# Optimization experiments

Measured on AMD Instinct MI355X. Metric: run time of the kernel, lower is better.

## Reference

```python
import jax, jax.numpy as jnp
import numpy as np

B, S, HID = 1, 2048, 2048
H = 16
DN, DR, DV = 128, 64, 128          # qk_nope_head_dim, qk_rope_head_dim, v_head_dim
DQ = DN + DR                        # q_head_dim = 192
QLR, KVLR = 1536, 512               # q_lora_rank, kv_lora_rank
MAXP = 32 * 1024
SCALE = DQ ** -0.5
EPS = 1e-6


def rmsnorm(x, w):
    return x * jax.lax.rsqrt(jnp.mean(x * x, axis=-1, keepdims=True) + EPS) * w


def rotate_half(x):
    h = x.shape[-1] // 2
    return jnp.concatenate((-x[..., h:], x[..., :h]), axis=-1)


def interleave_to_half(x):
    # torch: view(b,h,s,d//2,2).transpose(4,3).reshape(b,h,s,d)
    b, h, s, d = x.shape
    return x.reshape(b, h, s, d // 2, 2).transpose(0, 1, 2, 4, 3).reshape(b, h, s, d)


def setup_inputs() -> dict:
    key = jax.random.key(0)
    ks = jax.random.split(key, 8)
    def w(k, shape):
        fan_in = shape[-1]
        return jax.random.normal(k, shape, jnp.float32) * (fan_in ** -0.5)
    inp = {
        "hidden_states": jax.random.normal(ks[0], (B, S, HID), jnp.float32),
        "q_a_w": w(ks[1], (QLR, HID)),
        "q_a_ln": jnp.ones((QLR,), jnp.float32),
        "q_b_w": w(ks[2], (H * DQ, QLR)),
        "kv_a_w": w(ks[3], (KVLR + DR, HID)),
        "kv_a_ln": jnp.ones((KVLR,), jnp.float32),
        "kv_b_w": w(ks[4], (H * (DN + DV), KVLR)),
        "o_w": w(ks[5], (HID, H * DV)),
    }
    # rotary tables, seq_len = 32k
    inv_freq = 1.0 / (10000.0 ** (np.arange(0, DR, 2, dtype=np.float32) / DR))
    t = np.arange(MAXP, dtype=np.float32)
    freqs = np.outer(t, inv_freq)
    emb = np.concatenate((freqs, freqs), axis=-1)
    inp["cos"] = jnp.asarray(np.cos(emb), jnp.float32)
    inp["sin"] = jnp.asarray(np.sin(emb), jnp.float32)
    # bool mask, True = masked (causal)
    inp["attention_mask"] = jnp.triu(jnp.ones((S, S), bool), 1)[None, None]
    inp["position_ids"] = jnp.arange(S, dtype=jnp.int64 if jax.config.jax_enable_x64 else jnp.int32)[None].repeat(B, 0)
    return inp


def reference(hidden_states, q_a_w, q_a_ln, q_b_w, kv_a_w, kv_a_ln, kv_b_w, o_w,
              cos, sin, attention_mask, position_ids):
    b, s, _ = hidden_states.shape
    # low-rank Q: q_b(LN(q_a(x)))
    q = rmsnorm(hidden_states @ q_a_w.T, q_a_ln) @ q_b_w.T         # [b,s,H*DQ]
    q = q.reshape(b, s, H, DQ).transpose(0, 2, 1, 3)               # [b,H,s,DQ]
    q_nope, q_pe = q[..., :DN], q[..., DN:]
    # compressed KV + decoupled rope key
    ckv = hidden_states @ kv_a_w.T                                  # [b,s,KVLR+DR]
    compressed_kv, k_pe = ckv[..., :KVLR], ckv[..., KVLR:]
    k_pe = k_pe.reshape(b, s, 1, DR).transpose(0, 2, 1, 3)          # [b,1,s,DR]
    kv = rmsnorm(compressed_kv, kv_a_ln) @ kv_b_w.T                 # [b,s,H*(DN+DV)]
    kv = kv.reshape(b, s, H, DN + DV).transpose(0, 2, 1, 3)         # [b,H,s,DN+DV]
    k_nope, value_states = kv[..., :DN], kv[..., DN:]
    # rotary with interleaved->half reorder on the rope slice only
    cos_p = cos[position_ids][:, None]                              # [b,1,s,DR]
    sin_p = sin[position_ids][:, None]
    q_pe = interleave_to_half(q_pe)
    k_pe = interleave_to_half(k_pe)
    q_pe = q_pe * cos_p + rotate_half(q_pe) * sin_p
    k_pe = k_pe * cos_p + rotate_half(k_pe) * sin_p
    query_states = jnp.concatenate((q_nope, q_pe), axis=-1)         # [b,H,s,DQ]
    key_states = jnp.concatenate(
        (k_nope, jnp.broadcast_to(k_pe, (b, H, s, DR))), axis=-1)   # [b,H,s,DQ]
    # manual attention
    scores = jnp.einsum("bhqd,bhkd->bhqk", query_states, key_states) * SCALE
    scores = jnp.where(attention_mask, jnp.float32(-10000.0), scores)
    attn = jax.nn.softmax(scores.astype(jnp.float32), axis=-1).astype(query_states.dtype)
    attn_out = jnp.einsum("bhqk,bhkd->bhqd", attn, value_states)    # [b,H,s,DV]
    attn_out = attn_out.transpose(0, 2, 1, 3).reshape(b, s, H * DV)
    return attn_out @ o_w.T                                         # [b,s,HID]
```

## Files before the change

### kernel.cpp

```cpp
#include <hip/hip_runtime.h>
#include <stdint.h>

typedef unsigned short u16;
typedef __attribute__((ext_vector_type(8))) short short8;
typedef __attribute__((ext_vector_type(4))) float f32x4;
typedef __attribute__((ext_vector_type(4))) unsigned short ushort4_t;
typedef __attribute__((ext_vector_type(4))) float float4_t;

#define DEV_INLINE __device__ __forceinline__

DEV_INLINE u16 f2bf(float f) {
    union { float f; unsigned u; } x; x.f = f;
    unsigned u = x.u;
    unsigned r = (u + 0x7FFFu + ((u >> 16) & 1u)) >> 16;
    return (u16)r;
}

DEV_INLINE float fexp2(float x) {
    float r;
    asm("v_exp_f32 %0, %1" : "=v"(r) : "v"(x));
    return r;
}

DEV_INLINE unsigned cvtpk_bf16(float lo, float hi) {
    unsigned r;
    asm("v_cvt_pk_bf16_f32 %0, %1, %2" : "=v"(r) : "v"(lo), "v"(hi));
    return r;
}

template <int CTRL>
DEV_INLINE float dppmaxf(float x) {
    union { float f; int i; } u; u.f = x;
    int y = __builtin_amdgcn_update_dpp(u.i, u.i, CTRL, 0xf, 0xf, true);
    union { int i; float f; } v; v.i = y;
    return fmaxf(x, v.f);
}

DEV_INLINE float dpp_xor1(float x) {
    union { float f; int i; } u; u.f = x;
    int y = __builtin_amdgcn_update_dpp(u.i, u.i, 0xB1, 0xf, 0xf, true);
    union { int i; float f; } v; v.i = y;
    return v.f;
}

DEV_INLINE float rmax16(float x) {
    x = dppmaxf<0xB1>(x);
    x = dppmaxf<0x4E>(x);
    x = dppmaxf<0x141>(x);
    x = dppmaxf<0x140>(x);
    return x;
}

__global__ void conv_all(const float* __restrict__ s0, u16* __restrict__ d0, long e0,
                         const float* __restrict__ s1, u16* __restrict__ d1, long e1,
                         const float* __restrict__ s2, u16* __restrict__ d2, long e2,
                         const float* __restrict__ s3, u16* __restrict__ d3, long e3,
                         const float* __restrict__ s4, u16* __restrict__ d4, long e4,
                         const float* __restrict__ s5, u16* __restrict__ d5, long e5,
                         int rows_valid, int cols4) {
    long i = (long)blockIdx.x * 256 + threadIdx.x;
    if (i >= e5) return;
    if (i >= e4) {
        long j = i - e4;
        long row = j / cols4;
        ushort4_t o; o.x = 0; o.y = 0; o.z = 0; o.w = 0;
        if (row < rows_valid) {
            float4_t v = ((const float4_t*)s5)[j];
            o.x = f2bf(v.x); o.y = f2bf(v.y); o.z = f2bf(v.z); o.w = f2bf(v.w);
        }
        ((ushort4_t*)d5)[j] = o;
        return;
    }
    const float* s; u16* d; long base;
    if      (i < e0) { s = s0; d = d0; base = 0; }
    else if (i < e1) { s = s1; d = d1; base = e0; }
    else if (i < e2) { s = s2; d = d2; base = e1; }
    else if (i < e3) { s = s3; d = d3; base = e2; }
    else             { s = s4; d = d4; base = e3; }
    long j = i - base;
    float4_t v = ((const float4_t*)s)[j];
    ushort4_t o;
    o.x = f2bf(v.x); o.y = f2bf(v.y); o.z = f2bf(v.z); o.w = f2bf(v.w);
    ((ushort4_t*)d)[j] = o;
}

#define BK 32

DEV_INLINE void gload16(const u16* g, u16* l) {
    __builtin_amdgcn_global_load_lds((const __attribute__((address_space(1))) unsigned int*)g,
                                     (__attribute__((address_space(3))) unsigned int*)l,
                                     16, 0, 0);
}

template <typename OT>
__global__ __launch_bounds__(256) void gemm64_db(const u16* __restrict__ A, const u16* __restrict__ B,
                                                 OT* __restrict__ C, int M, int N, int K) {
    __shared__ u16 As[2][64 * BK];
    __shared__ u16 Bs[2][128 * BK];
    const int tid = threadIdx.x;
    const int wid = tid >> 6, lane = tid & 63;
    const int lm = lane & 15, lk = lane >> 4;
    const long bm = (long)blockIdx.y * 64, bn = (long)blockIdx.x * 128;

    f32x4 acc[4][2] = {};

    const int rowS = lane >> 2;
    const int colS = ((lane & 3) ^ ((lane >> 3) & 3)) * 8;
    const int cs = (lm >> 1) & 3;
    const u16* Ag = A + (bm + wid * 16 + rowS) * (long)K + colS;
    const u16* Bg = B + (bn + wid * 32 + rowS) * (long)K + colS;
    const int aoff = wid * 16 * BK;
    const int boff = wid * 32 * BK;

    gload16(Ag, &As[0][aoff]);
    gload16(Bg, &Bs[0][boff]);
    gload16(Bg + 16 * (long)K, &Bs[0][boff + 16 * BK]);
    __syncthreads();

    int cur = 0;
    for (int k0 = 0; k0 < K; k0 += BK) {
        if (k0 + BK < K) {
            gload16(Ag + k0 + BK, &As[cur ^ 1][aoff]);
            gload16(Bg + k0 + BK, &Bs[cur ^ 1][boff]);
            gload16(Bg + 16 * (long)K + k0 + BK, &Bs[cur ^ 1][boff + 16 * BK]);
        }
        short8 af[4], bfr[2];
#pragma unroll
        for (int m = 0; m < 4; ++m)
            af[m] = *(const short8*)&As[cur][(m * 16 + lm) * BK + (lk ^ cs) * 8];
#pragma unroll
        for (int n = 0; n < 2; ++n)
            bfr[n] = *(const short8*)&Bs[cur][(wid * 32 + n * 16 + lm) * BK + (lk ^ cs) * 8];
#pragma unroll
        for (int m = 0; m < 4; ++m)
#pragma unroll
            for (int n = 0; n < 2; ++n)
                acc[m][n] = __builtin_amdgcn_mfma_f32_16x16x32_bf16(af[m], bfr[n], acc[m][n], 0, 0, 0);
        __syncthreads();
        cur ^= 1;
    }

#pragma unroll
    for (int m = 0; m < 4; ++m)
#pragma unroll
        for (int n = 0; n < 2; ++n)
#pragma unroll
            for (int r = 0; r < 4; ++r) {
                long idx = (bm + m * 16 + lk * 4 + r) * (long)N + bn + wid * 32 + n * 16 + lm;
                if constexpr (sizeof(OT) == 4) C[idx] = acc[m][n][r];
                else                           C[idx] = f2bf(acc[m][n][r]);
            }
}

__global__ __launch_bounds__(256) void gemm_qkv(const u16* __restrict__ qnA, const u16* __restrict__ qbB,
                                                const u16* __restrict__ kvnA, const u16* __restrict__ kvbB,
                                                u16* __restrict__ Qb, u16* __restrict__ Kb, u16* __restrict__ Vt,
                                                const int* __restrict__ pos,
                                                const float* __restrict__ cosT, const float* __restrict__ sinT) {
    __shared__ u16 SMEM[12288];
    u16* As = SMEM;
    u16* Bs = SMEM + 4096;
    const int tid = threadIdx.x;
    const int wid = tid >> 6, lane = tid & 63;
    const int lm = lane & 15, lk = lane >> 4;

    const bool isq = blockIdx.x < 768;
    const int gx = isq ? blockIdx.x : blockIdx.x - 768;
    const int nb = isq ? 24 : 32;
    const int K  = isq ? 1536 : 512;
    const u16* A = isq ? qnA : kvnA;
    const u16* B = isq ? qbB : kvbB;
    const long bn = (long)(gx % nb) * 128;
    const long bm = (long)(gx / nb) * 64;

    f32x4 acc[4][2] = {};

    const int rowS = lane >> 2;
    const int colS = ((lane & 3) ^ ((lane >> 3) & 3)) * 8;
    const int cs = (lm >> 1) & 3;
    const u16* Ag = A + (bm + wid * 16 + rowS) * (long)K + colS;
    const u16* Bg = B + (bn + wid * 32 + rowS) * (long)K + colS;
    const int aoff = wid * 16 * BK;
    const int boff = wid * 32 * BK;

    gload16(Ag, &As[aoff]);
    gload16(Bg, &Bs[boff]);
    gload16(Bg + 16 * (long)K, &Bs[boff + 16 * BK]);
    __syncthreads();

    int cur = 0;
    for (int k0 = 0; k0 < K; k0 += BK) {
        if (k0 + BK < K) {
            gload16(Ag + k0 + BK, &As[(cur ^ 1) * 2048 + aoff]);
            gload16(Bg + k0 + BK, &Bs[(cur ^ 1) * 4096 + boff]);
            gload16(Bg + 16 * (long)K + k0 + BK, &Bs[(cur ^ 1) * 4096 + boff + 16 * BK]);
        }
        short8 af[4], bfr[2];
#pragma unroll
        for (int m = 0; m < 4; ++m)
            af[m] = *(const short8*)&As[cur * 2048 + (m * 16 + lm) * BK + (lk ^ cs) * 8];
#pragma unroll
        for (int n = 0; n < 2; ++n)
            bfr[n] = *(const short8*)&Bs[cur * 4096 + (wid * 32 + n * 16 + lm) * BK + (lk ^ cs) * 8];
#pragma unroll
        for (int m = 0; m < 4; ++m)
#pragma unroll
            for (int n = 0; n < 2; ++n)
                acc[m][n] = __builtin_amdgcn_mfma_f32_16x16x32_bf16(af[m], bfr[n], acc[m][n], 0, 0, 0);
        __syncthreads();
        cur ^= 1;
    }

    if (isq) {
#pragma unroll
        for (int n = 0; n < 2; ++n) {
            const int c = (int)bn + wid * 32 + n * 16 + lm;
            const int h = c / 192;
            const int d = c - h * 192;
            const bool pe = (d >= 128);
            const int t = (d - 128) >> 1;
#pragma unroll
            for (int m = 0; m < 4; ++m)
#pragma unroll
                for (int r = 0; r < 4; ++r) {
                    const long row = bm + m * 16 + lk * 4 + r;
                    float own = acc[m][n][r];
                    float par = dpp_xor1(own);
                    float val = own;
                    if (pe) {
                        long p = pos[row];
                        float cc = cosT[p * 64 + t];
                        float ss = sinT[p * 64 + t];
                        val = (d & 1) ? own * cc + par * ss : own * cc - par * ss;
                    }
                    Qb[((long)h * 2048 + row) * 192 + d] = f2bf(val);
                }
        }
    } else {
        const int hh = (gx & 31) >> 1;
        const bool isV = (gx & 1) != 0;
        if (!isV) {
#pragma unroll
            for (int m = 0; m < 4; ++m)
#pragma unroll
                for (int n = 0; n < 2; ++n)
#pragma unroll
                    for (int r = 0; r < 4; ++r)
                        Kb[((long)hh * 2048 + bm + m * 16 + lk * 4 + r) * 192 + wid * 32 + n * 16 + lm]
                            = f2bf(acc[m][n][r]);
        } else {
            __syncthreads();
            u16* Ls = SMEM;
#pragma unroll
            for (int n = 0; n < 2; ++n) {
                int d = wid * 32 + n * 16 + lm;
                int swz = ((d >> 3) & 7) << 3;
#pragma unroll
                for (int m = 0; m < 4; ++m)
#pragma unroll
                    for (int r = 0; r < 4; ++r) {
                        int row = m * 16 + lk * 4 + r;
                        Ls[d * 72 + (row ^ swz)] = f2bf(acc[m][n][r]);
                    }
            }
            __syncthreads();
#pragma unroll
            for (int i = 0; i < 8; ++i) {
                int u = i * 256 + tid;
                int d = u >> 4, s4 = (u & 15) * 4;
                int swz = ((d >> 3) & 7) << 3;
                ushort4_t v;
                v.x = Ls[d * 72 + ((s4 + 0) ^ swz)]; v.y = Ls[d * 72 + ((s4 + 1) ^ swz)];
                v.z = Ls[d * 72 + ((s4 + 2) ^ swz)]; v.w = Ls[d * 72 + ((s4 + 3) ^ swz)];
                *(ushort4_t*)(Vt + ((long)hh * 128 + d) * 2048 + bm + s4) = v;
            }
        }
    }
}

__global__ __launch_bounds__(256) void norm_rope(const float* __restrict__ qkva,
                                                 const float* __restrict__ q_ln,
                                                 const float* __restrict__ kv_ln,
                                                 u16* __restrict__ qn, u16* __restrict__ kvn,
                                                 const int* __restrict__ pos,
                                                 const float* __restrict__ cosT,
                                                 const float* __restrict__ sinT,
                                                 u16* __restrict__ Kb) {
    const int b = blockIdx.x, tid = threadIdx.x;
    if (b < 4096) {
        const bool isq = b < 2048;
        const int row = isq ? b : b - 2048;
        const int ncols = isq ? 1536 : 512;
        const float* x = qkva + (long)row * 2176 + (isq ? 0 : 1536);
        const float* w = isq ? q_ln : kv_ln;
        u16* out = isq ? (qn + (long)row * 1536) : (kvn + (long)row * 512);
        float ss = 0.f;
        for (int c = tid; c < ncols; c += 256) { float v = x[c]; ss = fmaf(v, v, ss); }
#pragma unroll
        for (int off = 32; off > 0; off >>= 1) ss += __shfl_down(ss, off);
        __shared__ float part[4];
        if ((tid & 63) == 0) part[tid >> 6] = ss;
        __syncthreads();
        float tot = part[0] + part[1] + part[2] + part[3];
        float rs = rsqrtf(tot / (float)ncols + 1e-6f);
        for (int c = tid; c < ncols; c += 256) out[c] = f2bf(x[c] * rs * w[c]);
    } else {
        int idx = (b - 4096) * 256 + tid;
        int s = idx >> 5, j = idx & 31;
        long p = pos[s];
        const float* row = qkva + (long)s * 2176 + 2048;
        float x0 = row[2 * j], x1 = row[2 * j + 1];
        float c0 = cosT[p * 64 + j], s0 = sinT[p * 64 + j];
        u16 o0 = f2bf(x0 * c0 - x1 * s0);
        u16 o1 = f2bf(x1 * c0 + x0 * s0);
#pragma unroll
        for (int h = 0; h < 16; ++h) {
            u16* kr = Kb + ((long)h * 2048 + s) * 192 + 128;
            kr[2 * j] = o0; kr[2 * j + 1] = o1;
        }
    }
}

__global__ __launch_bounds__(512) void attn_fwd(const u16* __restrict__ Qb, const u16* __restrict__ Kb,
                                                const u16* __restrict__ Vt, u16* __restrict__ Ao) {
    __shared__ __align__(16) char smem[51712];

    const int b = blockIdx.x;
    const int u = b & 255;
    const int h = (u & 7) * 2 + ((u >> 3) & 1);
    const int bq = u >> 4;
    const int qi = (b < 256) ? bq : 31 - bq;
    const int tid = threadIdx.x;
    const int wid = tid >> 6, lane = tid & 63;
    const int lm = lane & 15, lk = lane >> 4;
    const int s = wid >> 2, wp = wid & 3;
    const int t256 = tid & 255;

    u16* KsS = (u16*)smem + s * 6144;
    u16* VsS = (u16*)(smem + 24576) + s * 4096;
    u16* PsW = (u16*)(smem + 40960) + wid * 640;
    float* ML = (float*)(smem + 51200);
    float* Ob = (float*)smem;

    const u16* Kh = Kb + (long)h * 2048 * 192;
    const u16* Vh = Vt + (long)h * 128 * 2048;

    short8 bones = {};
    if (lm == 0) {
#pragma unroll
        for (int j = 0; j < 8; ++j) bones[j] = (short)0x3F80;
    }
    const float C2 = 0.104117548f;

    const int q0 = qi * 64;
    const int nt = 2 * qi + 2;
    const int niter = qi + 1;

    short8 qf[6];
    const u16* qbase = Qb + ((long)h * 2048 + q0 + wp * 16 + lm) * 192;
#pragma unroll
    for (int kf = 0; kf < 6; ++kf) qf[kf] = *(const short8*)(qbase + kf * 32 + lk * 8);

    f32x4 o[8] = {};
    f32x4 o9 = {};
    float mrow[4] = {-1e30f, -1e30f, -1e30f, -1e30f};

    short8 kreg[3], vreg[2];
    {
        const long k0 = s * 32;
#pragma unroll
        for (int i = 0; i < 3; ++i) {
            int idx = i * 256 + t256; int r = idx / 24, c = (idx % 24) * 8;
            kreg[i] = *(const short8*)(Kh + (k0 + r) * 192 + c);
        }
#pragma unroll
        for (int i = 0; i < 2; ++i) {
            int idx = i * 256 + t256; int dv = idx >> 2, kvb = idx & 3;
            vreg[i] = *(const short8*)(Vh + (long)dv * 2048 + k0 + kvb * 8);
        }
#pragma unroll
        for (int i = 0; i < 3; ++i) {
            int idx = i * 256 + t256; int r = idx / 24, c8 = idx % 24;
            *(short8*)&KsS[r * 192 + ((c8 ^ (r & 7)) << 3)] = kreg[i];
        }
#pragma unroll
        for (int i = 0; i < 2; ++i) {
            int idx = i * 256 + t256; int dv = idx >> 2, kvb = idx & 3;
            *(short8*)&VsS[kvb * 1024 + ((dv * 8) ^ (kvb * 16))] = vreg[i];
        }
    }
    __syncthreads();

    for (int it = 0; it < niter; ++it) {
        const int ts = 2 * it + s;
        const int k0 = ts * 32;
        const bool more = (it + 1 < niter);

        if (more) {
            const long k0n = (long)(ts + 2) * 32;
#pragma unroll
            for (int i = 0; i < 3; ++i) {
                int idx = i * 256 + t256; int r = idx / 24, c = (idx % 24) * 8;
                kreg[i] = *(const short8*)(Kh + (k0n + r) * 192 + c);
            }
#pragma unroll
            for (int i = 0; i < 2; ++i) {
                int idx = i * 256 + t256; int dv = idx >> 2, kvb = idx & 3;
                vreg[i] = *(const short8*)(Vh + (long)dv * 2048 + k0n + kvb * 8);
            }
        }

        f32x4 sfr[2] = {};
#pragma unroll
        for (int n = 0; n < 2; ++n)
#pragma unroll
            for (int kf = 0; kf < 6; ++kf) {
                short8 kb = *(const short8*)&KsS[(n * 16 + lm) * 192 + (((kf * 4 + lk) ^ (lm & 7)) << 3)];
                sfr[n] = __builtin_amdgcn_mfma_f32_16x16x32_bf16(qf[kf], kb, sfr[n], 0, 0, 0);
            }

        float sv[2][4];
        const bool bt = (ts >= nt - 2);
#pragma unroll
        for (int n = 0; n < 2; ++n)
#pragma unroll
            for (int r = 0; r < 4; ++r) {
                float val = sfr[n][r] * C2;
                if (bt && (k0 + n * 16 + lm > q0 + wp * 16 + lk * 4 + r)) val = -1e30f;
                sv[n][r] = val;
            }

        float pmax[4];
#pragma unroll
        for (int r = 0; r < 4; ++r)
            pmax[r] = rmax16(fmaxf(sv[0][r], sv[1][r]));
        bool need = (pmax[0] > mrow[0] + 8.f) || (pmax[1] > mrow[1] + 8.f) ||
                    (pmax[2] > mrow[2] + 8.f) || (pmax[3] > mrow[3] + 8.f);
        if (__any(need)) {
#pragma unroll
            for (int r = 0; r < 4; ++r) {
                float mnew = fmaxf(mrow[r], pmax[r]);
                float alpha = fexp2(mrow[r] - mnew);
                mrow[r] = mnew;
#pragma unroll
                for (int d = 0; d < 8; ++d) o[d][r] *= alpha;
                o9[r] *= alpha;
            }
        }
#pragma unroll
        for (int n = 0; n < 2; ++n) {
            float p0 = fexp2(sv[n][0] - mrow[0]);
            float p1 = fexp2(sv[n][1] - mrow[1]);
            float p2 = fexp2(sv[n][2] - mrow[2]);
            float p3 = fexp2(sv[n][3] - mrow[3]);
            unsigned pk01 = cvtpk_bf16(p0, p1);
            unsigned pk23 = cvtpk_bf16(p2, p3);
            int rb = (lk * 4) * 40 + n * 16 + lm;
            PsW[rb]       = (u16)pk01;
            PsW[rb + 40]  = (u16)(pk01 >> 16);
            PsW[rb + 80]  = (u16)pk23;
            PsW[rb + 120] = (u16)(pk23 >> 16);
        }

        short8 pf = *(const short8*)&PsW[lm * 40 + lk * 8];
#pragma unroll
        for (int d = 0; d < 8; ++d) {
            short8 vf = *(const short8*)&VsS[lk * 1024 + (((d * 16 + lm) * 8) ^ (lk * 16))];
            o[d] = __builtin_amdgcn_mfma_f32_16x16x32_bf16(pf, vf, o[d], 0, 0, 0);
        }
        o9 = __builtin_amdgcn_mfma_f32_16x16x32_bf16(pf, bones, o9, 0, 0, 0);

        __syncthreads();
        if (more) {
#pragma unroll
            for (int i = 0; i < 3; ++i) {
                int idx = i * 256 + t256; int r = idx / 24, c8 = idx % 24;
                *(short8*)&KsS[r * 192 + ((c8 ^ (r & 7)) << 3)] = kreg[i];
            }
#pragma unroll
            for (int i = 0; i < 2; ++i) {
                int idx = i * 256 + t256; int dv = idx >> 2, kvb = idx & 3;
                *(short8*)&VsS[kvb * 1024 + ((dv * 8) ^ (kvb * 16))] = vreg[i];
            }
        }
        __syncthreads();
    }

    if (s == 1) {
#pragma unroll
        for (int d = 0; d < 8; ++d)
#pragma unroll
            for (int r = 0; r < 4; ++r)
                Ob[(wp * 16 + lk * 4 + r) * 128 + d * 16 + lm] = o[d][r];
        if (lm == 0) {
#pragma unroll
            for (int r = 0; r < 4; ++r) {
                int row = wp * 16 + lk * 4 + r;
                ML[row * 2 + 0] = mrow[r];
                ML[row * 2 + 1] = o9[r];
            }
        }
    }
    __syncthreads();
    if (s == 0) {
        float e0[4], e1[4], invl[4];
#pragma unroll
        for (int r = 0; r < 4; ++r) {
            int row = wp * 16 + lk * 4 + r;
            float m1 = ML[row * 2 + 0];
            float l1 = ML[row * 2 + 1];
            float l0 = __shfl(o9[r], lane & 48);
            float M = fmaxf(mrow[r], m1);
            e0[r] = fexp2(mrow[r] - M);
            e1[r] = fexp2(m1 - M);
            invl[r] = 1.f / (l0 * e0[r] + l1 * e1[r]);
        }
#pragma unroll
        for (int d = 0; d < 8; ++d)
#pragma unroll
            for (int r = 0; r < 4; ++r) {
                int row = wp * 16 + lk * 4 + r;
                float val = (o[d][r] * e0[r] +
                             Ob[row * 128 + d * 16 + lm] * e1[r]) * invl[r];
                Ao[((long)q0 + row) * 2048 + h * 128 + d * 16 + lm] = f2bf(val);
            }
    }
}

extern "C" void kernel_launch(void* const* d_in, const int* in_sizes, int n_in,
                              void* d_out, int out_size, void* d_ws, size_t ws_size,
                              hipStream_t stream) {
    (void)in_sizes; (void)n_in; (void)out_size; (void)ws_size;
    const float* hidden  = (const float*)d_in[0];
    const float* q_a_w   = (const float*)d_in[1];
    const float* q_a_ln  = (const float*)d_in[2];
    const float* q_b_w   = (const float*)d_in[3];
    const float* kv_a_w  = (const float*)d_in[4];
    const float* kv_a_ln = (const float*)d_in[5];
    const float* kv_b_w  = (const float*)d_in[6];
    const float* o_w     = (const float*)d_in[7];
    const float* cosT    = (const float*)d_in[8];
    const float* sinT    = (const float*)d_in[9];
    const int*   pos     = (const int*)d_in[11];

    char* ws = (char*)d_ws;
    u16* o_w_bf   = (u16*)(ws + 0);
    u16* qb_w_bf  = (u16*)(ws + 8388608);
    u16* kvb_w_bf = (u16*)(ws + 17825792);
    u16* qn_bf    = (u16*)(ws + 22020096);
    u16* kvn_bf   = (u16*)(ws + 28311552);
    u16* Qb       = (u16*)(ws + 30408704);
    u16* Kb       = (u16*)(ws + 42991616);
    u16* Vt       = (u16*)(ws + 55574528);
    u16* aout_bf  = (u16*)(ws + 63963136);
    u16*   hid_bf    = (u16*)(ws + 72351744);
    u16*   qkva_w_bf = (u16*)(ws + 80740352);
    float* qkva_f    = (float*)(ws + 89653248);

    conv_all<<<19200, 256, 0, stream>>>(
        hidden, hid_bf,                 1048576L,
        q_a_w,  qkva_w_bf,              1835008L,
        q_b_w,  qb_w_bf,                3014656L,
        kv_b_w, kvb_w_bf,               3538944L,
        o_w,    o_w_bf,                 4587520L,
        kv_a_w, qkva_w_bf + 1536L*2048, 4915200L,
        576, 512);

    gemm64_db<float><<<dim3(17, 32), 256, 0, stream>>>(hid_bf, qkva_w_bf, qkva_f, 2048, 2176, 2048);

    norm_rope<<<4352, 256, 0, stream>>>(qkva_f, q_a_ln, kv_a_ln, qn_bf, kvn_bf, pos, cosT, sinT, Kb);

    gemm_qkv<<<1792, 256, 0, stream>>>(qn_bf, qb_w_bf, kvn_bf, kvb_w_bf, Qb, Kb, Vt, pos, cosT, sinT);

    attn_fwd<<<512, 512, 0, stream>>>(Qb, Kb, Vt, aout_bf);

    gemm64_db<float><<<dim3(16, 32), 256, 0, stream>>>(aout_bf, o_w_bf, (float*)d_out, 2048, 2048, 2048);
}
```

Measured before the change: 224.2 us.

## Restructure attention into 4-way KV split with paired causal q-tiles per block

The attention kernel now launches 256 blocks, and each block handles two q-tiles (qi and 31-qi) one after the other to balance causal work. Each block splits the KV range four ways, and each wave computes 32 query rows so every loaded K/V fragment feeds two MFMAs. The four partial softmax states are combined through a two-level tree in shared memory. This raises LDS use to about 101 KB per block, which likely limits a CU to one resident block and adds extra reduction syncs.

New measurement: 310.4 us, median of 2. 38.5% more time.

```diff
diff --git a/kernel.cpp b/kernel.cpp
--- a/kernel.cpp
+++ b/kernel.cpp
@@ -323,24 +323,24 @@
 
 __global__ __launch_bounds__(512) void attn_fwd(const u16* __restrict__ Qb, const u16* __restrict__ Kb,
                                                 const u16* __restrict__ Vt, u16* __restrict__ Ao) {
-    __shared__ __align__(16) char smem[51712];
+    __shared__ __align__(16) char smem[103424];
 
     const int b = blockIdx.x;
-    const int u = b & 255;
-    const int h = (u & 7) * 2 + ((u >> 3) & 1);
-    const int bq = u >> 4;
-    const int qi = (b < 256) ? bq : 31 - bq;
+    const int h = (b & 7) * 2 + ((b >> 3) & 1);
+    const int pi = b >> 4;
     const int tid = threadIdx.x;
     const int wid = tid >> 6, lane = tid & 63;
     const int lm = lane & 15, lk = lane >> 4;
-    const int s = wid >> 2, wp = wid & 3;
-    const int t256 = tid & 255;
-
-    u16* KsS = (u16*)smem + s * 6144;
-    u16* VsS = (u16*)(smem + 24576) + s * 4096;
-    u16* PsW = (u16*)(smem + 40960) + wid * 640;
-    float* ML = (float*)(smem + 51200);
-    float* Ob = (float*)smem;
+    const int s = wid >> 1, wq = wid & 1;
+    const int t128 = tid & 127;
+
+    u16* KsS = (u16*)(smem + s * 20480);
+    u16* VsS = (u16*)(smem + s * 20480 + 12288);
+    u16* PsW = (u16*)(smem + 81920) + wid * 1280;
+    float* MLa = (float*)(smem + 102400);
+    float* MLb = (float*)(smem + 102912);
+    float* BUF0 = (float*)smem;
+    float* BUF1 = (float*)(smem + 32768);
 
     const u16* Kh = Kb + (long)h * 2048 * 192;
     const u16* Vh = Vt + (long)h * 128 * 2048;
@@ -352,178 +352,266 @@
     }
     const float C2 = 0.104117548f;
 
-    const int q0 = qi * 64;
-    const int nt = 2 * qi + 2;
-    const int niter = qi + 1;
-
-    short8 qf[6];
-    const u16* qbase = Qb + ((long)h * 2048 + q0 + wp * 16 + lm) * 192;
-#pragma unroll
-    for (int kf = 0; kf < 6; ++kf) qf[kf] = *(const short8*)(qbase + kf * 32 + lk * 8);
-
-    f32x4 o[8] = {};
-    f32x4 o9 = {};
-    float mrow[4] = {-1e30f, -1e30f, -1e30f, -1e30f};
-
-    short8 kreg[3], vreg[2];
-    {
-        const long k0 = s * 32;
-#pragma unroll
-        for (int i = 0; i < 3; ++i) {
-            int idx = i * 256 + t256; int r = idx / 24, c = (idx % 24) * 8;
-            kreg[i] = *(const short8*)(Kh + (k0 + r) * 192 + c);
-        }
-#pragma unroll
-        for (int i = 0; i < 2; ++i) {
-            int idx = i * 256 + t256; int dv = idx >> 2, kvb = idx & 3;
-            vreg[i] = *(const short8*)(Vh + (long)dv * 2048 + k0 + kvb * 8);
-        }
-#pragma unroll
-        for (int i = 0; i < 3; ++i) {
-            int idx = i * 256 + t256; int r = idx / 24, c8 = idx % 24;
-            *(short8*)&KsS[r * 192 + ((c8 ^ (r & 7)) << 3)] = kreg[i];
-        }
-#pragma unroll
-        for (int i = 0; i < 2; ++i) {
-            int idx = i * 256 + t256; int dv = idx >> 2, kvb = idx & 3;
-            *(short8*)&VsS[kvb * 1024 + ((dv * 8) ^ (kvb * 16))] = vreg[i];
-        }
-    }
-    __syncthreads();
-
-    for (int it = 0; it < niter; ++it) {
-        const int ts = 2 * it + s;
-        const int k0 = ts * 32;
-        const bool more = (it + 1 < niter);
-
-        if (more) {
-            const long k0n = (long)(ts + 2) * 32;
-#pragma unroll
-            for (int i = 0; i < 3; ++i) {
-                int idx = i * 256 + t256; int r = idx / 24, c = (idx % 24) * 8;
-                kreg[i] = *(const short8*)(Kh + (k0n + r) * 192 + c);
-            }
-#pragma unroll
-            for (int i = 0; i < 2; ++i) {
-                int idx = i * 256 + t256; int dv = idx >> 2, kvb = idx & 3;
-                vreg[i] = *(const short8*)(Vh + (long)dv * 2048 + k0n + kvb * 8);
-            }
-        }
-
-        f32x4 sfr[2] = {};
-#pragma unroll
-        for (int n = 0; n < 2; ++n)
-#pragma unroll
-            for (int kf = 0; kf < 6; ++kf) {
-                short8 kb = *(const short8*)&KsS[(n * 16 + lm) * 192 + (((kf * 4 + lk) ^ (lm & 7)) << 3)];
-                sfr[n] = __builtin_amdgcn_mfma_f32_16x16x32_bf16(qf[kf], kb, sfr[n], 0, 0, 0);
-            }
-
-        float sv[2][4];
-        const bool bt = (ts >= nt - 2);
-#pragma unroll
-        for (int n = 0; n < 2; ++n)
-#pragma unroll
-            for (int r = 0; r < 4; ++r) {
-                float val = sfr[n][r] * C2;
-                if (bt && (k0 + n * 16 + lm > q0 + wp * 16 + lk * 4 + r)) val = -1e30f;
-                sv[n][r] = val;
-            }
-
-        float pmax[4];
-#pragma unroll
-        for (int r = 0; r < 4; ++r)
-            pmax[r] = rmax16(fmaxf(sv[0][r], sv[1][r]));
-        bool need = (pmax[0] > mrow[0] + 8.f) || (pmax[1] > mrow[1] + 8.f) ||
-                    (pmax[2] > mrow[2] + 8.f) || (pmax[3] > mrow[3] + 8.f);
-        if (__any(need)) {
-#pragma unroll
-            for (int r = 0; r < 4; ++r) {
-                float mnew = fmaxf(mrow[r], pmax[r]);
-                float alpha = fexp2(mrow[r] - mnew);
-                mrow[r] = mnew;
-#pragma unroll
-                for (int d = 0; d < 8; ++d) o[d][r] *= alpha;
-                o9[r] *= alpha;
-            }
-        }
-#pragma unroll
-        for (int n = 0; n < 2; ++n) {
-            float p0 = fexp2(sv[n][0] - mrow[0]);
-            float p1 = fexp2(sv[n][1] - mrow[1]);
-            float p2 = fexp2(sv[n][2] - mrow[2]);
-            float p3 = fexp2(sv[n][3] - mrow[3]);
-            unsigned pk01 = cvtpk_bf16(p0, p1);
-            unsigned pk23 = cvtpk_bf16(p2, p3);
-            int rb = (lk * 4) * 40 + n * 16 + lm;
-            PsW[rb]       = (u16)pk01;
-            PsW[rb + 40]  = (u16)(pk01 >> 16);
-            PsW[rb + 80]  = (u16)pk23;
-            PsW[rb + 120] = (u16)(pk23 >> 16);
-        }
-
-        short8 pf = *(const short8*)&PsW[lm * 40 + lk * 8];
-#pragma unroll
-        for (int d = 0; d < 8; ++d) {
-            short8 vf = *(const short8*)&VsS[lk * 1024 + (((d * 16 + lm) * 8) ^ (lk * 16))];
-            o[d] = __builtin_amdgcn_mfma_f32_16x16x32_bf16(pf, vf, o[d], 0, 0, 0);
-        }
-        o9 = __builtin_amdgcn_mfma_f32_16x16x32_bf16(pf, bones, o9, 0, 0, 0);
-
-        __syncthreads();
-        if (more) {
-#pragma unroll
-            for (int i = 0; i < 3; ++i) {
-                int idx = i * 256 + t256; int r = idx / 24, c8 = idx % 24;
-                *(short8*)&KsS[r * 192 + ((c8 ^ (r & 7)) << 3)] = kreg[i];
-            }
-#pragma unroll
-            for (int i = 0; i < 2; ++i) {
-                int idx = i * 256 + t256; int dv = idx >> 2, kvb = idx & 3;
-                *(short8*)&VsS[kvb * 1024 + ((dv * 8) ^ (kvb * 16))] = vreg[i];
-            }
-        }
-        __syncthreads();
-    }
-
-    if (s == 1) {
-#pragma unroll
-        for (int d = 0; d < 8; ++d)
-#pragma unroll
-            for (int r = 0; r < 4; ++r)
-                Ob[(wp * 16 + lk * 4 + r) * 128 + d * 16 + lm] = o[d][r];
-        if (lm == 0) {
-#pragma unroll
-            for (int r = 0; r < 4; ++r) {
-                int row = wp * 16 + lk * 4 + r;
-                ML[row * 2 + 0] = mrow[r];
-                ML[row * 2 + 1] = o9[r];
-            }
-        }
-    }
-    __syncthreads();
-    if (s == 0) {
-        float e0[4], e1[4], invl[4];
-#pragma unroll
-        for (int r = 0; r < 4; ++r) {
-            int row = wp * 16 + lk * 4 + r;
-            float m1 = ML[row * 2 + 0];
-            float l1 = ML[row * 2 + 1];
-            float l0 = __shfl(o9[r], lane & 48);
-            float M = fmaxf(mrow[r], m1);
-            e0[r] = fexp2(mrow[r] - M);
-            e1[r] = fexp2(m1 - M);
-            invl[r] = 1.f / (l0 * e0[r] + l1 * e1[r]);
-        }
-#pragma unroll
-        for (int d = 0; d < 8; ++d)
-#pragma unroll
-            for (int r = 0; r < 4; ++r) {
-                int row = wp * 16 + lk * 4 + r;
-                float val = (o[d][r] * e0[r] +
-                             Ob[row * 128 + d * 16 + lm] * e1[r]) * invl[r];
-                Ao[((long)q0 + row) * 2048 + h * 128 + d * 16 + lm] = f2bf(val);
-            }
+    for (int half = 0; half < 2; ++half) {
+        const int qi = half ? (31 - pi) : pi;
+        const int q0 = qi * 64;
+        const int nt = 2 * (qi + 1);
+        const int L = (nt + 3) >> 2;
+
+        short8 qf[2][6];
+#pragma unroll
+        for (int mg = 0; mg < 2; ++mg) {
+            const u16* qbase = Qb + ((long)h * 2048 + q0 + wq * 32 + mg * 16 + lm) * 192;
+#pragma unroll
+            for (int kf = 0; kf < 6; ++kf) qf[mg][kf] = *(const short8*)(qbase + kf * 32 + lk * 8);
+        }
+
+        f32x4 o[2][8] = {};
+        f32x4 o9[2] = {};
+        float mrow[2][4] = {{-1e30f, -1e30f, -1e30f, -1e30f}, {-1e30f, -1e30f, -1e30f, -1e30f}};
+
+        short8 kreg[6], vreg[4];
+        {
+            const bool act0 = (s < nt);
+            const long k0 = (long)s * 32;
+            if (act0) {
+#pragma unroll
+                for (int i = 0; i < 6; ++i) {
+                    int idx = i * 128 + t128; int r = idx / 24, c = (idx % 24) * 8;
+                    kreg[i] = *(const short8*)(Kh + (k0 + r) * 192 + c);
+                }
+#pragma unroll
+                for (int i = 0; i < 4; ++i) {
+                    int idx = i * 128 + t128; int dv = idx >> 2, kvb = idx & 3;
+                    vreg[i] = *(const short8*)(Vh + (long)dv * 2048 + k0 + kvb * 8);
+                }
+#pragma unroll
+                for (int i = 0; i < 6; ++i) {
+                    int idx = i * 128 + t128; int r = idx / 24, c8 = idx % 24;
+                    *(short8*)&KsS[r * 192 + ((c8 ^ (r & 7)) << 3)] = kreg[i];
+                }
+#pragma unroll
+                for (int i = 0; i < 4; ++i) {
+                    int idx = i * 128 + t128; int dv = idx >> 2, kvb = idx & 3;
+                    *(short8*)&VsS[kvb * 1024 + ((dv * 8) ^ (kvb * 16))] = vreg[i];
+                }
+            }
+        }
+        __syncthreads();
+
+        for (int it = 0; it < L; ++it) {
+            const int ts = 4 * it + s;
+            const int k0 = ts * 32;
+            const bool active = (ts < nt);
+            const int ts_n = ts + 4;
+            const bool next_act = (ts_n < nt);
+
+            if (next_act) {
+                const long k0n = (long)ts_n * 32;
+#pragma unroll
+                for (int i = 0; i < 6; ++i) {
+                    int idx = i * 128 + t128; int r = idx / 24, c = (idx % 24) * 8;
+                    kreg[i] = *(const short8*)(Kh + (k0n + r) * 192 + c);
+                }
+#pragma unroll
+                for (int i = 0; i < 4; ++i) {
+                    int idx = i * 128 + t128; int dv = idx >> 2, kvb = idx & 3;
+                    vreg[i] = *(const short8*)(Vh + (long)dv * 2048 + k0n + kvb * 8);
+                }
+            }
+
+            if (active) {
+                f32x4 sfr[2][2] = {};
+#pragma unroll
+                for (int kf = 0; kf < 6; ++kf)
+#pragma unroll
+                    for (int n = 0; n < 2; ++n) {
+                        short8 kb = *(const short8*)&KsS[(n * 16 + lm) * 192 + (((kf * 4 + lk) ^ (lm & 7)) << 3)];
+#pragma unroll
+                        for (int mg = 0; mg < 2; ++mg)
+                            sfr[mg][n] = __builtin_amdgcn_mfma_f32_16x16x32_bf16(qf[mg][kf], kb, sfr[mg][n], 0, 0, 0);
+                    }
+
+                float sv[2][2][4];
+                const bool bt = (ts >= nt - 2);
+#pragma unroll
+                for (int mg = 0; mg < 2; ++mg)
+#pragma unroll
+                    for (int n = 0; n < 2; ++n)
+#pragma unroll
+                        for (int r = 0; r < 4; ++r) {
+                            float val = sfr[mg][n][r] * C2;
+                            if (bt && (k0 + n * 16 + lm > q0 + wq * 32 + mg * 16 + lk * 4 + r)) val = -1e30f;
+                            sv[mg][n][r] = val;
+                        }
+
+                float pmax[2][4];
+#pragma unroll
+                for (int mg = 0; mg < 2; ++mg)
+#pragma unroll
+                    for (int r = 0; r < 4; ++r)
+                        pmax[mg][r] = rmax16(fmaxf(sv[mg][0][r], sv[mg][1][r]));
+                bool need = false;
+#pragma unroll
+                for (int mg = 0; mg < 2; ++mg)
+#pragma unroll
+                    for (int r = 0; r < 4; ++r) need = need || (pmax[mg][r] > mrow[mg][r] + 8.f);
+                if (__any(need)) {
+#pragma unroll
+                    for (int mg = 0; mg < 2; ++mg)
+#pragma unroll
+                        for (int r = 0; r < 4; ++r) {
+                            float mnew = fmaxf(mrow[mg][r], pmax[mg][r]);
+                            float alpha = fexp2(mrow[mg][r] - mnew);
+                            mrow[mg][r] = mnew;
+#pragma unroll
+                            for (int d = 0; d < 8; ++d) o[mg][d][r] *= alpha;
+                            o9[mg][r] *= alpha;
+                        }
+                }
+#pragma unroll
+                for (int mg = 0; mg < 2; ++mg)
+#pragma unroll
+                    for (int n = 0; n < 2; ++n) {
+                        float p0 = fexp2(sv[mg][n][0] - mrow[mg][0]);
+                        float p1 = fexp2(sv[mg][n][1] - mrow[mg][1]);
+                        float p2 = fexp2(sv[mg][n][2] - mrow[mg][2]);
+                        float p3 = fexp2(sv[mg][n][3] - mrow[mg][3]);
+                        unsigned pk01 = cvtpk_bf16(p0, p1);
+                        unsigned pk23 = cvtpk_bf16(p2, p3);
+                        int rb = (mg * 16 + lk * 4) * 40 + n * 16 + lm;
+                        PsW[rb]       = (u16)pk01;
+                        PsW[rb + 40]  = (u16)(pk01 >> 16);
+                        PsW[rb + 80]  = (u16)pk23;
+                        PsW[rb + 120] = (u16)(pk23 >> 16);
+                    }
+
+                short8 pf0 = *(const short8*)&PsW[lm * 40 + lk * 8];
+                short8 pf1 = *(const short8*)&PsW[(16 + lm) * 40 + lk * 8];
+#pragma unroll
+                for (int d = 0; d < 8; ++d) {
+                    short8 vf = *(const short8*)&VsS[lk * 1024 + (((d * 16 + lm) * 8) ^ (lk * 16))];
+                    o[0][d] = __builtin_amdgcn_mfma_f32_16x16x32_bf16(pf0, vf, o[0][d], 0, 0, 0);
+                    o[1][d] = __builtin_amdgcn_mfma_f32_16x16x32_bf16(pf1, vf, o[1][d], 0, 0, 0);
+                }
+                o9[0] = __builtin_amdgcn_mfma_f32_16x16x32_bf16(pf0, bones, o9[0], 0, 0, 0);
+                o9[1] = __builtin_amdgcn_mfma_f32_16x16x32_bf16(pf1, bones, o9[1], 0, 0, 0);
+            }
+
+            __syncthreads();
+            if (next_act) {
+#pragma unroll
+                for (int i = 0; i < 6; ++i) {
+                    int idx = i * 128 + t128; int r = idx / 24, c8 = idx % 24;
+                    *(short8*)&KsS[r * 192 + ((c8 ^ (r & 7)) << 3)] = kreg[i];
+                }
+#pragma unroll
+                for (int i = 0; i < 4; ++i) {
+                    int idx = i * 128 + t128; int dv = idx >> 2, kvb = idx & 3;
+                    *(short8*)&VsS[kvb * 1024 + ((dv * 8) ^ (kvb * 16))] = vreg[i];
+                }
+            }
+            __syncthreads();
+        }
+
+        if (s >= 2) {
+            float* B = (s == 2) ? BUF0 : BUF1;
+            float* ML = (s == 2) ? MLa : MLb;
+#pragma unroll
+            for (int mg = 0; mg < 2; ++mg)
+#pragma unroll
+                for (int d = 0; d < 8; ++d)
+#pragma unroll
+                    for (int r = 0; r < 4; ++r)
+                        B[(wq * 32 + mg * 16 + lk * 4 + r) * 128 + d * 16 + lm] = o[mg][d][r];
+            if (lm == 0) {
+#pragma unroll
+                for (int mg = 0; mg < 2; ++mg)
+#pragma unroll
+                    for (int r = 0; r < 4; ++r) {
+                        int row = wq * 32 + mg * 16 + lk * 4 + r;
+                        ML[row * 2 + 0] = mrow[mg][r];
+                        ML[row * 2 + 1] = o9[mg][r];
+                    }
+            }
+        }
+        __syncthreads();
+        if (s <= 1) {
+            float* B = (s == 0) ? BUF0 : BUF1;
+            float* ML = (s == 0) ? MLa : MLb;
+            float e0[2][4], e1[2][4];
+#pragma unroll
+            for (int mg = 0; mg < 2; ++mg)
+#pragma unroll
+                for (int r = 0; r < 4; ++r) {
+                    int row = wq * 32 + mg * 16 + lk * 4 + r;
+                    float m1 = ML[row * 2 + 0];
+                    float l1 = ML[row * 2 + 1];
+                    float M = fmaxf(mrow[mg][r], m1);
+                    e0[mg][r] = fexp2(mrow[mg][r] - M);
+                    e1[mg][r] = fexp2(m1 - M);
+                    mrow[mg][r] = M;
+                    o9[mg][r] = o9[mg][r] * e0[mg][r] + l1 * e1[mg][r];
+                }
+#pragma unroll
+            for (int mg = 0; mg < 2; ++mg)
+#pragma unroll
+                for (int d = 0; d < 8; ++d)
+#pragma unroll
+                    for (int r = 0; r < 4; ++r) {
+                        int row = wq * 32 + mg * 16 + lk * 4 + r;
+                        o[mg][d][r] = o[mg][d][r] * e0[mg][r] + B[row * 128 + d * 16 + lm] * e1[mg][r];
+                    }
+        }
+        __syncthreads();
+        if (s == 1) {
+#pragma unroll
+            for (int mg = 0; mg < 2; ++mg)
+#pragma unroll
+                for (int d = 0; d < 8; ++d)
+#pragma unroll
+                    for (int r = 0; r < 4; ++r)
+                        BUF0[(wq * 32 + mg * 16 + lk * 4 + r) * 128 + d * 16 + lm] = o[mg][d][r];
+            if (lm == 0) {
+#pragma unroll
+                for (int mg = 0; mg < 2; ++mg)
+#pragma unroll
+                    for (int r = 0; r < 4; ++r) {
+                        int row = wq * 32 + mg * 16 + lk * 4 + r;
+                        MLa[row * 2 + 0] = mrow[mg][r];
+                        MLa[row * 2 + 1] = o9[mg][r];
+                    }
+            }
+        }
+        __syncthreads();
+        if (s == 0) {
+            float e0[2][4], e1[2][4], invl[2][4];
+#pragma unroll
+            for (int mg = 0; mg < 2; ++mg)
+#pragma unroll
+                for (int r = 0; r < 4; ++r) {
+                    int row = wq * 32 + mg * 16 + lk * 4 + r;
+                    float m1 = MLa[row * 2 + 0];
+                    float l1 = MLa[row * 2 + 1];
+                    float l0 = __shfl(o9[mg][r], lane & 48);
+                    float M = fmaxf(mrow[mg][r], m1);
+                    e0[mg][r] = fexp2(mrow[mg][r] - M);
+                    e1[mg][r] = fexp2(m1 - M);
+                    invl[mg][r] = 1.f / (l0 * e0[mg][r] + l1 * e1[mg][r]);
+                }
+#pragma unroll
+            for (int mg = 0; mg < 2; ++mg)
+#pragma unroll
+                for (int d = 0; d < 8; ++d)
+#pragma unroll
+                    for (int r = 0; r < 4; ++r) {
+                        int row = wq * 32 + mg * 16 + lk * 4 + r;
+                        float val = (o[mg][d][r] * e0[mg][r] +
+                                     BUF0[row * 128 + d * 16 + lm] * e1[mg][r]) * invl[mg][r];
+                        Ao[((long)q0 + row) * 2048 + h * 128 + d * 16 + lm] = f2bf(val);
+                    }
+        }
+        __syncthreads();
     }
 }
 
@@ -572,7 +660,7 @@
 
     gemm_qkv<<<1792, 256, 0, stream>>>(qn_bf, qb_w_bf, kvn_bf, kvb_w_bf, Qb, Kb, Vt, pos, cosT, sinT);
 
-    attn_fwd<<<512, 512, 0, stream>>>(Qb, Kb, Vt, aout_bf);
+    attn_fwd<<<256, 512, 0, stream>>>(Qb, Kb, Vt, aout_bf);
 
     gemm64_db<float><<<dim3(16, 32), 256, 0, stream>>>(aout_bf, o_w_bf, (float*)d_out, 2048, 2048, 2048);
 }
```
